# Performance work log

Measured on AMD Instinct MI355X. Metric: run time of the kernel, lower is better.

Reference implementation:

```python
import jax, jax.numpy as jnp
import numpy as np

HEADS = 16
DHEAD = 128
B, S, DMODEL = 2, 2048, 2048


def setup_inputs() -> dict:
    key = jax.random.key(0)
    k1, k2, k3 = jax.random.split(key, 3)
    x = jax.random.normal(k1, (B, S, DMODEL), dtype=jnp.float32)
    # Linear weights, stored as [in, out] so forward is x @ w (no bias).
    w_in = jax.random.normal(k2, (DMODEL, 3 * HEADS * DHEAD), dtype=jnp.float32) * (DMODEL ** -0.5)
    w_out = jax.random.normal(k3, (HEADS * DHEAD, DMODEL), dtype=jnp.float32) * ((HEADS * DHEAD) ** -0.5)
    # Causal mask: True = masked (strictly upper triangular), broadcast over batch & heads.
    mask = jnp.triu(jnp.ones((S, S), dtype=jnp.bool_), k=1)[None, None, :, :]
    return {"x": x, "w_in": w_in, "w_out": w_out, "mask": mask}


def reference(x, w_in, w_out, mask):
    b, s, _ = x.shape
    # Fused QKV projection: [b,s,3*H*dh] -> [b,s,H,3*dh] -> chunk into q,k,v [b,s,H,dh]
    projected = (x @ w_in).reshape(b, s, HEADS, 3 * DHEAD)
    q, k, v = jnp.split(projected, 3, axis=-1)
    # Scores [b,H,l,L], scaled by 1/sqrt(dhead)
    scale = 1.0 / (DHEAD ** 0.5)
    a = jnp.einsum("blhd,bLhd->bhlL", q, k) * scale
    a = jnp.where(mask, -jnp.inf, a)
    a = jax.nn.softmax(a, axis=-1)
    # Weighted values -> [b,l,H,dh] -> flatten heads -> output projection
    out = jnp.einsum("bhlL,bLhd->blhd", a, v).reshape(b, s, HEADS * DHEAD)
    return out @ w_out
```

## Files before the change

### kernel.cpp

```cpp
#include <hip/hip_runtime.h>

#define HD    16
#define DH    128
#define BB    2
#define SS    2048
#define DM    2048
#define NQKV  6144
#define MTOT  4096

typedef short   bfx8  __attribute__((ext_vector_type(8)));
typedef float   f32x4 __attribute__((ext_vector_type(4)));

__device__ __forceinline__ unsigned short f2bf(float f) {
  union { float f; unsigned int u; } c; c.f = f;
  unsigned int u = c.u + 0x7FFFu + ((c.u >> 16) & 1u);
  return (unsigned short)(u >> 16);
}

__device__ __forceinline__ void gload_lds16(const unsigned short* g, unsigned short* l) {
  __builtin_amdgcn_global_load_lds(
      (const __attribute__((address_space(1))) unsigned int*)g,
      (__attribute__((address_space(3))) unsigned int*)l, 16, 0, 0);
}

#define BARS() do { __builtin_amdgcn_sched_barrier(0); __builtin_amdgcn_s_barrier(); \
                    __builtin_amdgcn_sched_barrier(0); } while (0)
#define VMCNT7() do { asm volatile("s_waitcnt vmcnt(7)" ::: "memory"); \
                      __builtin_amdgcn_sched_barrier(0); } while (0)
#define VMCNT6() do { asm volatile("s_waitcnt vmcnt(6)" ::: "memory"); \
                      __builtin_amdgcn_sched_barrier(0); } while (0)

__global__ __launch_bounds__(256) void f32_to_bf16_k(const float* __restrict__ in,
                                                     unsigned short* __restrict__ out, int n4) {
  int i = (blockIdx.x * 256 + threadIdx.x);
  if (i >= n4) return;
  const float4 v = *(const float4*)(in + (size_t)i * 4);
  ushort4 o;
  o.x = f2bf(v.x); o.y = f2bf(v.y); o.z = f2bf(v.z); o.w = f2bf(v.w);
  *(ushort4*)(out + (size_t)i * 4) = o;
}

__global__ __launch_bounds__(256) void transpose_f32_bf16_k(const float* __restrict__ in,
                                                            unsigned short* __restrict__ out,
                                                            int R, int C) {
  __shared__ float t[32][33];
  const int c0 = blockIdx.x * 32, r0 = blockIdx.y * 32;
  const int tx = threadIdx.x & 31, ty = threadIdx.x >> 5;
#pragma unroll
  for (int i = 0; i < 4; i++) {
    int r = r0 + ty + i * 8;
    t[ty + i * 8][tx] = in[(size_t)r * C + c0 + tx];
  }
  __syncthreads();
#pragma unroll
  for (int i = 0; i < 4; i++) {
    int c = c0 + ty + i * 8;
    out[(size_t)c * R + r0 + tx] = f2bf(t[tx][ty + i * 8]);
  }
}

__global__ __launch_bounds__(512, 2) void gemm256_qkv_k(const unsigned short* __restrict__ A,
                                                        const unsigned short* __restrict__ Bt,
                                                        unsigned short* __restrict__ Qg,
                                                        unsigned short* __restrict__ Kg,
                                                        unsigned short* __restrict__ Vg,
                                                        int K) {
  __shared__ __align__(16) unsigned short Asb[2][256 * 64];
  __shared__ __align__(16) unsigned short Bsb[2][192 * 64];
  const int tid = threadIdx.x;
  const int lane = tid & 63, wid = tid >> 6;
  const int wr = wid >> 2, wc = wid & 3;
  const int cbase = lane & 15, rgrp = lane >> 4;
  const int bid = (int)blockIdx.x;
  const int id = (bid & 7) * 64 + (bid >> 3);
  const int nb = id >> 4, mb = id & 15;
  const size_t m0 = (size_t)mb * 256, n0 = (size_t)nb * 192;
  const int nkt = K >> 6;

#define STAGE_A64(u_, g_) do {                                                          \
    const int uc_ = ((u_) < nkt ? (u_) : (nkt - 1));                                    \
    const int r_ = tid >> 3, s_ = tid & 7;                                              \
    gload_lds16(A + (m0 + (g_) * 64 + r_) * (size_t)K + uc_ * 64 +                      \
                    (((s_ * 16) ^ ((r_ & 7) << 4)) >> 1),                               \
                &Asb[(u_) & 1][(g_) * 4096] + tid * 8); } while (0)
#define STAGE_B64(u_, g_) do {                                                          \
    const int uc_ = ((u_) < nkt ? (u_) : (nkt - 1));                                    \
    const int r_ = tid >> 3, s_ = tid & 7;                                              \
    gload_lds16(Bt + (n0 + (g_) * 64 + r_) * (size_t)K + uc_ * 64 +                     \
                    (((s_ * 16) ^ ((r_ & 7) << 4)) >> 1),                               \
                &Bsb[(u_) & 1][(g_) * 4096] + tid * 8); } while (0)

  const int axor = (cbase & 7) << 4;
  int a_off[2], b_off[2];
#pragma unroll
  for (int ks = 0; ks < 2; ks++) {
    a_off[ks] = ((wr * 128 + cbase) * 128 + ((ks * 64 + rgrp * 16) ^ axor)) >> 1;
    b_off[ks] = ((wc * 48 + cbase) * 128 + ((ks * 64 + rgrp * 16) ^ axor)) >> 1;
  }

#define RD_A03(dst_, p_) do { _Pragma("unroll")                                          \
    for (int mf_ = 0; mf_ < 4; mf_++) { _Pragma("unroll")                                \
      for (int ks_ = 0; ks_ < 2; ks_++)                                                  \
        dst_[mf_][ks_] = *(const bfx8*)((p_) + a_off[ks_] + mf_ * 1024); } } while (0)
#define RD_A47(dst_, p_) do { _Pragma("unroll")                                          \
    for (int mf_ = 0; mf_ < 4; mf_++) { _Pragma("unroll")                                \
      for (int ks_ = 0; ks_ < 2; ks_++)                                                  \
        dst_[mf_][ks_] = *(const bfx8*)((p_) + a_off[ks_] + (mf_ + 4) * 1024); } } while (0)
#define RD_B01(dst_, p_) do { _Pragma("unroll")                                          \
    for (int nf_ = 0; nf_ < 2; nf_++) { _Pragma("unroll")                                \
      for (int ks_ = 0; ks_ < 2; ks_++)                                                  \
        dst_[nf_][ks_] = *(const bfx8*)((p_) + b_off[ks_] + nf_ * 1024); } } while (0)
#define RD_B2(dst_, p_) do { _Pragma("unroll")                                           \
    for (int ks_ = 0; ks_ < 2; ks_++)                                                    \
      dst_[0][ks_] = *(const bfx8*)((p_) + b_off[ks_] + 2 * 1024); } while (0)

#define MFMA_2N(mo_, AF_, BF_) do {                                                      \
    __builtin_amdgcn_s_setprio(1);                                                      \
    _Pragma("unroll")                                                                    \
    for (int mf_ = 0; mf_ < 4; mf_++) { _Pragma("unroll")                                \
      for (int nf_ = 0; nf_ < 2; nf_++) { _Pragma("unroll")                              \
        for (int ks_ = 0; ks_ < 2; ks_++)                                                \
          acc[mf_ + (mo_)][nf_] = __builtin_amdgcn_mfma_f32_16x16x32_bf16(               \
              AF_[mf_][ks_], BF_[nf_][ks_], acc[mf_ + (mo_)][nf_], 0, 0, 0); } }         \
    __builtin_amdgcn_s_setprio(0); } while (0)

  f32x4 acc[8][3];
  const f32x4 z = {0.f, 0.f, 0.f, 0.f};
#pragma unroll
  for (int mf = 0; mf < 8; mf++)
#pragma unroll
    for (int nf = 0; nf < 3; nf++) acc[mf][nf] = z;

  STAGE_A64(0, 0); STAGE_A64(0, 1); STAGE_A64(0, 2); STAGE_A64(0, 3);
  STAGE_B64(0, 0); STAGE_B64(0, 1); STAGE_B64(0, 2);
  STAGE_A64(1, 0); STAGE_A64(1, 1); STAGE_A64(1, 2); STAGE_A64(1, 3);
  STAGE_B64(1, 0); STAGE_B64(1, 1); STAGE_B64(1, 2);
  VMCNT7();
  BARS();
  bfx8 a03A[4][2], b01A[2][2], a03B[4][2], b01B[2][2];
  RD_A03(a03A, &Asb[0][0]);
  RD_B01(b01A, &Bsb[0][0]);

#define TILE_BODY(u_, A03c, B01c, A03n, B01n) do {                                       \
    const unsigned short* As_  = &Asb[(u_) & 1][0];                                      \
    const unsigned short* Bs_  = &Bsb[(u_) & 1][0];                                      \
    const unsigned short* Asn_ = &Asb[((u_) + 1) & 1][0];                                \
    const unsigned short* Bsn_ = &Bsb[((u_) + 1) & 1][0];                                \
    bfx8 a47[4][2], b2[1][2];                                                            \
    RD_A47(a47, As_);                                                                    \
    STAGE_A64((u_) + 2, 0); STAGE_A64((u_) + 2, 2);                                      \
    BARS();                                                                              \
    MFMA_2N(0, A03c, B01c);                                                              \
    RD_B2(b2, Bs_);                                                                      \
    STAGE_A64((u_) + 2, 1); STAGE_A64((u_) + 2, 3);                                      \
    BARS();                                                                              \
    MFMA_2N(4, a47, B01c);                                                               \
    STAGE_B64((u_) + 2, 0); STAGE_B64((u_) + 2, 1); STAGE_B64((u_) + 2, 2);              \
    VMCNT7();                                                                            \
    BARS();                                                                              \
    RD_A03(A03n, Asn_);                                                                  \
    RD_B01(B01n, Bsn_);                                                                  \
    __builtin_amdgcn_s_setprio(1);                                                      \
    _Pragma("unroll")                                                                    \
    for (int mf_ = 0; mf_ < 4; mf_++) { _Pragma("unroll")                                \
      for (int ks_ = 0; ks_ < 2; ks_++) {                                                \
        acc[mf_][2] = __builtin_amdgcn_mfma_f32_16x16x32_bf16(                           \
            A03c[mf_][ks_], b2[0][ks_], acc[mf_][2], 0, 0, 0);                           \
        acc[mf_ + 4][2] = __builtin_amdgcn_mfma_f32_16x16x32_bf16(                       \
            a47[mf_][ks_], b2[0][ks_], acc[mf_ + 4][2], 0, 0, 0);                        \
      } }                                                                                \
    __builtin_amdgcn_s_setprio(0);                                                      \
    BARS();                                                                              \
  } while (0)

#pragma unroll 1
  for (int u = 0; u < nkt; u += 2) {
    TILE_BODY(u,     a03A, b01A, a03B, b01B);
    TILE_BODY(u + 1, a03B, b01B, a03A, b01A);
  }
#undef TILE_BODY
#undef STAGE_A64
#undef STAGE_B64

#pragma unroll
  for (int mf = 0; mf < 8; mf++)
#pragma unroll
    for (int nf = 0; nf < 3; nf++) {
      const int nn = (int)n0 + wc * 48 + nf * 16;
      const int h = nn / 384, tt = (nn >> 7) % 3;
      const int d = (nn & 127) + cbase;
      const int row0 = (int)m0 + wr * 128 + mf * 16 + rgrp * 4;
      const int bb = row0 >> 11;
      const int s0 = row0 & 2047;
      if (tt == 2) {
        ushort4 v;
        v.x = f2bf(acc[mf][nf][0]); v.y = f2bf(acc[mf][nf][1]);
        v.z = f2bf(acc[mf][nf][2]); v.w = f2bf(acc[mf][nf][3]);
        *(ushort4*)(Vg + ((size_t)(bb * HD + h) * DH + d) * SS + s0) = v;
      } else {
        unsigned short* dst = (tt == 0 ? Qg : Kg);
#pragma unroll
        for (int r = 0; r < 4; r++)
          dst[((size_t)(bb * HD + h) * SS + s0 + r) * DH + d] = f2bf(acc[mf][nf][r]);
      }
    }
}

__global__ __launch_bounds__(512, 2) void gemm256_out_k(const unsigned short* __restrict__ A,
                                                        const unsigned short* __restrict__ Bt,
                                                        float* __restrict__ C, int K, int ldc) {
  __shared__ __align__(16) unsigned short Asb[2][256 * 64];
  __shared__ __align__(16) unsigned short Bsb[2][128 * 64];
  const int tid = threadIdx.x;
  const int lane = tid & 63, wid = tid >> 6;
  const int wr = wid >> 2, wc = wid & 3;
  const int cbase = lane & 15, rgrp = lane >> 4;
  const int bid = (int)blockIdx.x;
  const int id = (bid & 7) * 32 + (bid >> 3);
  const int nb = id >> 4, mb = id & 15;
  const size_t m0 = (size_t)mb * 256, n0 = (size_t)nb * 128;
  const int nkt = K >> 6;

#define STAGE_AO(u_, g_) do {                                                           \
    const int uc_ = ((u_) < nkt ? (u_) : (nkt - 1));                                    \
    const int r_ = tid >> 3, s_ = tid & 7;                                              \
    gload_lds16(A + (m0 + (g_) * 64 + r_) * (size_t)K + uc_ * 64 +                      \
                    (((s_ * 16) ^ ((r_ & 7) << 4)) >> 1),                               \
                &Asb[(u_) & 1][(g_) * 4096] + tid * 8); } while (0)
#define STAGE_BO(u_, g_) do {                                                           \
    const int uc_ = ((u_) < nkt ? (u_) : (nkt - 1));                                    \
    const int r_ = tid >> 3, s_ = tid & 7;                                              \
    gload_lds16(Bt + (n0 + (g_) * 64 + r_) * (size_t)K + uc_ * 64 +                     \
                    (((s_ * 16) ^ ((r_ & 7) << 4)) >> 1),                               \
                &Bsb[(u_) & 1][(g_) * 4096] + tid * 8); } while (0)

  const int axor = (cbase & 7) << 4;
  int a_off[2], b_off[2];
#pragma unroll
  for (int ks = 0; ks < 2; ks++) {
    a_off[ks] = ((wr * 128 + cbase) * 128 + ((ks * 64 + rgrp * 16) ^ axor)) >> 1;
    b_off[ks] = ((wc * 32 + cbase) * 128 + ((ks * 64 + rgrp * 16) ^ axor)) >> 1;
  }

#define MFMA_O(mo_, AF_, BF_) do {                                                       \
    __builtin_amdgcn_s_setprio(1);                                                      \
    _Pragma("unroll")                                                                    \
    for (int mf_ = 0; mf_ < 4; mf_++) { _Pragma("unroll")                                \
      for (int nf_ = 0; nf_ < 2; nf_++) { _Pragma("unroll")                              \
        for (int ks_ = 0; ks_ < 2; ks_++)                                                \
          acc[mf_ + (mo_)][nf_] = __builtin_amdgcn_mfma_f32_16x16x32_bf16(               \
              AF_[mf_][ks_], BF_[nf_][ks_], acc[mf_ + (mo_)][nf_], 0, 0, 0); } }         \
    __builtin_amdgcn_s_setprio(0); } while (0)

  f32x4 acc[8][2];
  const f32x4 z = {0.f, 0.f, 0.f, 0.f};
#pragma unroll
  for (int mf = 0; mf < 8; mf++)
#pragma unroll
    for (int nf = 0; nf < 2; nf++) acc[mf][nf] = z;

  STAGE_AO(0, 0); STAGE_AO(0, 1); STAGE_AO(0, 2); STAGE_AO(0, 3);
  STAGE_BO(0, 0); STAGE_BO(0, 1);
  STAGE_AO(1, 0); STAGE_AO(1, 1); STAGE_AO(1, 2); STAGE_AO(1, 3);
  STAGE_BO(1, 0); STAGE_BO(1, 1);
  VMCNT6();
  BARS();
  bfx8 a03A[4][2], b01A[2][2], a03B[4][2], b01B[2][2];
  RD_A03(a03A, &Asb[0][0]);
  RD_B01(b01A, &Bsb[0][0]);

#define TILE_BODY_O(u_, A03c, B01c, A03n, B01n) do {                                     \
    const unsigned short* As_  = &Asb[(u_) & 1][0];                                      \
    const unsigned short* Bs_  = &Bsb[(u_) & 1][0];                                      \
    const unsigned short* Asn_ = &Asb[((u_) + 1) & 1][0];                                \
    const unsigned short* Bsn_ = &Bsb[((u_) + 1) & 1][0];                                \
    bfx8 a47[4][2];                                                                      \
    \
    RD_A47(a47, As_);                                                                    \
    STAGE_AO((u_) + 2, 0); STAGE_AO((u_) + 2, 2);                                        \
    BARS();                                                                              \
    MFMA_O(0, A03c, B01c);                                                               \
     \
               \
    STAGE_AO((u_) + 2, 1); STAGE_AO((u_) + 2, 3);                                        \
    STAGE_BO((u_) + 2, 0); STAGE_BO((u_) + 2, 1);                                        \
    VMCNT6();                                                                            \
    BARS();                                                                              \
    RD_A03(A03n, Asn_);                                                                  \
    RD_B01(B01n, Bsn_);                                                                  \
    MFMA_O(4, a47, B01c);                                                                \
    BARS();                                                                              \
  } while (0)

#pragma unroll 1
  for (int u = 0; u < nkt; u += 2) {
    TILE_BODY_O(u,     a03A, b01A, a03B, b01B);
    TILE_BODY_O(u + 1, a03B, b01B, a03A, b01A);
  }
#undef TILE_BODY_O
#undef STAGE_AO
#undef STAGE_BO

#pragma unroll
  for (int mf = 0; mf < 8; mf++)
#pragma unroll
    for (int nf = 0; nf < 2; nf++)
#pragma unroll
      for (int r = 0; r < 4; r++) {
        size_t row = m0 + wr * 128 + mf * 16 + rgrp * 4 + r;
        size_t col = n0 + wc * 32 + nf * 16 + cbase;
        C[row * ldc + col] = acc[mf][nf][r];
      }
}

__global__ __launch_bounds__(256) void attn_fwd_k(const unsigned short* __restrict__ Qg,
                                                  const unsigned short* __restrict__ Kg,
                                                  const unsigned short* __restrict__ Vg,
                                                  unsigned short* __restrict__ ao) {
  __shared__ __align__(16) unsigned short Klds[2][64 * 128];
  __shared__ __align__(16) unsigned short Vt[2][128 * 64];
  __shared__ __align__(16) unsigned short Plds[4][16 * 64];
  const int tid = threadIdx.x;
  const int lane = tid & 63, wid = tid >> 6;
  const int cbase = lane & 15, rgrp = lane >> 4;
  const int cx = (cbase & 7) << 4;

  const int bid = (int)blockIdx.x;
  const int bh = (bid & 7) * 4 + ((bid >> 3) & 3);
  const int qt = 31 - (bid >> 5);
  const int b = bh >> 4, h = bh & 15;
  const int qbase = qt * 64;

  const unsigned short* qp0 = Qg + (size_t)(b * HD + h) * SS * DH;
  const unsigned short* kp  = Kg + (size_t)(b * HD + h) * SS * DH;
  const unsigned short* vp  = Vg + (size_t)(b * HD + h) * DH * SS;
  const float scale = 0.08838834764831845f;
  const f32x4 z = {0.f, 0.f, 0.f, 0.f};
  const int qi = qbase + wid * 16 + cbase;

  bfx8 qf[4];
  {
    const unsigned short* qp = qp0 + (size_t)qi * DH;
#pragma unroll
    for (int ks = 0; ks < 4; ks++) qf[ks] = *(const bfx8*)(qp + ks * 32 + rgrp * 8);
  }

  float m_run = -1e30f, l_run = 0.f;
  f32x4 o[8];
#pragma unroll
  for (int mb = 0; mb < 8; mb++) o[mb] = z;

#define STAGE_T(t_, s_) do {                                                        \
    const int kvb_ = (t_) * 64;                                                     \
    _Pragma("unroll")                                                               \
    for (int i_ = 0; i_ < 4; i_++) {                                                \
      int idx_ = i_ * 256 + tid;                                                    \
      int r_ = idx_ >> 4, bo_ = (idx_ & 15) * 16;                                   \
      gload_lds16(kp + (size_t)(kvb_ + r_) * DH + ((bo_ ^ ((r_ & 7) << 4)) >> 1),   \
                  &Klds[s_][idx_ * 8]);                                             \
    }                                                                               \
    _Pragma("unroll")                                                               \
    for (int i_ = 0; i_ < 4; i_++) {                                                \
      int idx_ = i_ * 256 + tid;                                                    \
      int d_ = idx_ >> 3, bo_ = (idx_ & 7) * 16;                                    \
      gload_lds16(vp + (size_t)d_ * SS + kvb_ + ((bo_ ^ ((d_ & 7) << 4)) >> 1),     \
                  &Vt[s_][idx_ * 8]);                                               \
    } } while (0)

  const int ntiles = qt + 1;
  STAGE_T(0, 0);
  __syncthreads();

  for (int t = 0; t < ntiles; ++t) {
    const int sel = t & 1;
    if (t + 1 < ntiles) STAGE_T(t + 1, sel ^ 1);
    const unsigned short* Ks_ = &Klds[sel][0];
    const unsigned short* Vs_ = &Vt[sel][0];
    const int kvb = t * 64;

    f32x4 s[4];
#pragma unroll
    for (int mf = 0; mf < 4; mf++) s[mf] = z;
#pragma unroll
    for (int mf = 0; mf < 4; mf++)
#pragma unroll
      for (int ks = 0; ks < 4; ks++) {
        bfx8 kf = *(const bfx8*)(Ks_ + (((mf * 16 + cbase) * 256 + ((ks * 64 + rgrp * 16) ^ cx)) >> 1));
        s[mf] = __builtin_amdgcn_mfma_f32_16x16x32_bf16(kf, qf[ks], s[mf], 0, 0, 0);
      }

    float sv[4][4];
    const bool diag = (t == ntiles - 1);
#pragma unroll
    for (int mf = 0; mf < 4; mf++)
#pragma unroll
      for (int r = 0; r < 4; r++) {
        float v = s[mf][r] * scale;
        if (diag && (kvb + mf * 16 + rgrp * 4 + r > qi)) v = -1e30f;
        sv[mf][r] = v;
      }
    float tm = sv[0][0];
#pragma unroll
    for (int mf = 0; mf < 4; mf++)
#pragma unroll
      for (int r = 0; r < 4; r++) tm = fmaxf(tm, sv[mf][r]);
    tm = fmaxf(tm, __shfl_xor(tm, 16));
    tm = fmaxf(tm, __shfl_xor(tm, 32));
    const float mnew = fmaxf(m_run, tm);
    float p[4][4];
    float rs = 0.f;
#pragma unroll
    for (int mf = 0; mf < 4; mf++)
#pragma unroll
      for (int r = 0; r < 4; r++) { p[mf][r] = __expf(sv[mf][r] - mnew); rs += p[mf][r]; }
    rs += __shfl_xor(rs, 16);
    rs += __shfl_xor(rs, 32);
    const float alpha = __expf(m_run - mnew);
    l_run = l_run * alpha + rs;
    m_run = mnew;
#pragma unroll
    for (int mb = 0; mb < 8; mb++)
#pragma unroll
      for (int r = 0; r < 4; r++) o[mb][r] *= alpha;

#pragma unroll
    for (int mf = 0; mf < 4; mf++)
#pragma unroll
      for (int rr = 0; rr < 2; rr++) {
        unsigned int pp = (unsigned int)f2bf(p[mf][2 * rr]) |
                          ((unsigned int)f2bf(p[mf][2 * rr + 1]) << 16);
        *(unsigned int*)((char*)&Plds[wid][0] +
                         (cbase * 128 + ((mf * 32 + rgrp * 8 + rr * 4) ^ cx))) = pp;
      }
    bfx8 pf[2];
#pragma unroll
    for (int k2 = 0; k2 < 2; k2++)
      pf[k2] = *(const bfx8*)((const char*)&Plds[wid][0] +
                              (cbase * 128 + ((k2 * 64 + rgrp * 16) ^ cx)));

#pragma unroll
    for (int mb = 0; mb < 8; mb++)
#pragma unroll
      for (int k2 = 0; k2 < 2; k2++) {
        bfx8 vf = *(const bfx8*)(Vs_ + (((mb * 16 + cbase) * 128 + ((k2 * 64 + rgrp * 16) ^ cx)) >> 1));
        o[mb] = __builtin_amdgcn_mfma_f32_16x16x32_bf16(vf, pf[k2], o[mb], 0, 0, 0);
      }
    __syncthreads();
  }
#undef STAGE_T

  const float rinv = 1.0f / l_run;
  unsigned short* aop = ao + ((size_t)(b * SS + qi)) * DM + h * DH + rgrp * 4;
#pragma unroll
  for (int mb = 0; mb < 8; mb++) {
    ushort4 v;
    v.x = f2bf(o[mb][0] * rinv); v.y = f2bf(o[mb][1] * rinv);
    v.z = f2bf(o[mb][2] * rinv); v.w = f2bf(o[mb][3] * rinv);
    *(ushort4*)(aop + mb * 16) = v;
  }
}

extern "C" void kernel_launch(void* const* d_in, const int* in_sizes, int n_in,
                              void* d_out, int out_size, void* d_ws, size_t ws_size,
                              hipStream_t stream) {
  (void)in_sizes; (void)n_in; (void)out_size; (void)ws_size;
  const float* x     = (const float*)d_in[0];
  const float* w_in  = (const float*)d_in[1];
  const float* w_out = (const float*)d_in[2];
  float* out = (float*)d_out;

  char* ws = (char*)d_ws;
  unsigned short* Xb  = (unsigned short*)(ws);
  unsigned short* Wit = (unsigned short*)(ws + (16ull << 20));
  unsigned short* Wot = (unsigned short*)(ws + (40ull << 20));
  unsigned short* Qg  = (unsigned short*)(ws + (48ull << 20));
  unsigned short* Kg  = (unsigned short*)(ws + (64ull << 20));
  unsigned short* Vg  = (unsigned short*)(ws + (80ull << 20));
  unsigned short* AO  = (unsigned short*)(ws + (96ull << 20));

  f32_to_bf16_k<<<MTOT * DM / 4 / 256, 256, 0, stream>>>(x, Xb, MTOT * DM / 4);
  transpose_f32_bf16_k<<<dim3(NQKV / 32, DM / 32), 256, 0, stream>>>(w_in, Wit, DM, NQKV);
  transpose_f32_bf16_k<<<dim3(DM / 32, DM / 32), 256, 0, stream>>>(w_out, Wot, DM, DM);
  gemm256_qkv_k<<<512, 512, 0, stream>>>(Xb, Wit, Qg, Kg, Vg, DM);
  attn_fwd_k<<<1024, 256, 0, stream>>>(Qg, Kg, Vg, AO);
  gemm256_out_k<<<256, 512, 0, stream>>>(AO, Wot, out, DM, DM);
}
```

Before: 235.2 us.

## Process 128 query rows per attention block, two 16-row groups per wave

The attention kernel now handles a 128-row query tile per block, with each wave computing two 16-row query groups that share every K and V fragment read from LDS. This halves the number of blocks and the K/V global-to-LDS staging per query row, and doubles MFMA work per LDS fragment load. Waves skip KV tiles past their own causal boundary, and masking is applied per group. The cost is roughly double the accumulator registers (launch bounds now request 2 blocks per SM), fewer blocks for load balancing, and some waves idling at the diagonal tiles.

```diff
diff --git a/kernel.cpp b/kernel.cpp
--- a/kernel.cpp
+++ b/kernel.cpp
@@ -275,13 +275,10 @@
     const unsigned short* Asn_ = &Asb[((u_) + 1) & 1][0];                                \
     const unsigned short* Bsn_ = &Bsb[((u_) + 1) & 1][0];                                \
     bfx8 a47[4][2];                                                                      \
-    \
     RD_A47(a47, As_);                                                                    \
     STAGE_AO((u_) + 2, 0); STAGE_AO((u_) + 2, 2);                                        \
     BARS();                                                                              \
     MFMA_O(0, A03c, B01c);                                                               \
-     \
-               \
     STAGE_AO((u_) + 2, 1); STAGE_AO((u_) + 2, 3);                                        \
     STAGE_BO((u_) + 2, 0); STAGE_BO((u_) + 2, 1);                                        \
     VMCNT6();                                                                            \
@@ -313,13 +310,13 @@
       }
 }
 
-__global__ __launch_bounds__(256) void attn_fwd_k(const unsigned short* __restrict__ Qg,
-                                                  const unsigned short* __restrict__ Kg,
-                                                  const unsigned short* __restrict__ Vg,
-                                                  unsigned short* __restrict__ ao) {
+__global__ __launch_bounds__(256, 2) void attn_fwd_k(const unsigned short* __restrict__ Qg,
+                                                     const unsigned short* __restrict__ Kg,
+                                                     const unsigned short* __restrict__ Vg,
+                                                     unsigned short* __restrict__ ao) {
   __shared__ __align__(16) unsigned short Klds[2][64 * 128];
   __shared__ __align__(16) unsigned short Vt[2][128 * 64];
-  __shared__ __align__(16) unsigned short Plds[4][16 * 64];
+  __shared__ __align__(16) unsigned short Plds[4][2][16 * 64];
   const int tid = threadIdx.x;
   const int lane = tid & 63, wid = tid >> 6;
   const int cbase = lane & 15, rgrp = lane >> 4;
@@ -327,28 +324,36 @@
 
   const int bid = (int)blockIdx.x;
   const int bh = (bid & 7) * 4 + ((bid >> 3) & 3);
-  const int qt = 31 - (bid >> 5);
+  const int qt = 15 - (bid >> 5);
   const int b = bh >> 4, h = bh & 15;
-  const int qbase = qt * 64;
+  const int qbase = qt * 128;
 
   const unsigned short* qp0 = Qg + (size_t)(b * HD + h) * SS * DH;
   const unsigned short* kp  = Kg + (size_t)(b * HD + h) * SS * DH;
   const unsigned short* vp  = Vg + (size_t)(b * HD + h) * DH * SS;
   const float scale = 0.08838834764831845f;
   const f32x4 z = {0.f, 0.f, 0.f, 0.f};
-  const int qi = qbase + wid * 16 + cbase;
-
-  bfx8 qf[4];
-  {
-    const unsigned short* qp = qp0 + (size_t)qi * DH;
-#pragma unroll
-    for (int ks = 0; ks < 4; ks++) qf[ks] = *(const bfx8*)(qp + ks * 32 + rgrp * 8);
-  }
-
-  float m_run = -1e30f, l_run = 0.f;
-  f32x4 o[8];
-#pragma unroll
-  for (int mb = 0; mb < 8; mb++) o[mb] = z;
+  const int q0 = qbase + wid * 32;
+  const int qend = q0 + 32;
+  int qi[2];
+  qi[0] = q0 + cbase; qi[1] = q0 + 16 + cbase;
+
+  bfx8 qf[2][4];
+#pragma unroll
+  for (int g = 0; g < 2; g++) {
+    const unsigned short* qp = qp0 + (size_t)qi[g] * DH;
+#pragma unroll
+    for (int ks = 0; ks < 4; ks++) qf[g][ks] = *(const bfx8*)(qp + ks * 32 + rgrp * 8);
+  }
+
+  float m_run[2], l_run[2];
+  f32x4 o[2][8];
+#pragma unroll
+  for (int g = 0; g < 2; g++) {
+    m_run[g] = -1e30f; l_run[g] = 0.f;
+#pragma unroll
+    for (int mb = 0; mb < 8; mb++) o[g][mb] = z;
+  }
 
 #define STAGE_T(t_, s_) do {                                                        \
     const int kvb_ = (t_) * 64;                                                     \
@@ -367,7 +372,7 @@
                   &Vt[s_][idx_ * 8]);                                               \
     } } while (0)
 
-  const int ntiles = qt + 1;
+  const int ntiles = (qbase >> 6) + 2;
   STAGE_T(0, 0);
   __syncthreads();
 
@@ -378,85 +383,100 @@
     const unsigned short* Vs_ = &Vt[sel][0];
     const int kvb = t * 64;
 
-    f32x4 s[4];
-#pragma unroll
-    for (int mf = 0; mf < 4; mf++) s[mf] = z;
-#pragma unroll
-    for (int mf = 0; mf < 4; mf++)
-#pragma unroll
-      for (int ks = 0; ks < 4; ks++) {
-        bfx8 kf = *(const bfx8*)(Ks_ + (((mf * 16 + cbase) * 256 + ((ks * 64 + rgrp * 16) ^ cx)) >> 1));
-        s[mf] = __builtin_amdgcn_mfma_f32_16x16x32_bf16(kf, qf[ks], s[mf], 0, 0, 0);
+    if (kvb < qend) {
+      f32x4 s[2][4];
+#pragma unroll
+      for (int g = 0; g < 2; g++)
+#pragma unroll
+        for (int mf = 0; mf < 4; mf++) s[g][mf] = z;
+#pragma unroll
+      for (int mf = 0; mf < 4; mf++)
+#pragma unroll
+        for (int ks = 0; ks < 4; ks++) {
+          bfx8 kf = *(const bfx8*)(Ks_ + (((mf * 16 + cbase) * 256 + ((ks * 64 + rgrp * 16) ^ cx)) >> 1));
+          s[0][mf] = __builtin_amdgcn_mfma_f32_16x16x32_bf16(kf, qf[0][ks], s[0][mf], 0, 0, 0);
+          s[1][mf] = __builtin_amdgcn_mfma_f32_16x16x32_bf16(kf, qf[1][ks], s[1][mf], 0, 0, 0);
+        }
+
+      float p[2][4][4];
+#pragma unroll
+      for (int g = 0; g < 2; g++) {
+        float sv[4][4];
+        const bool maskable = (kvb + 64 > q0 + g * 16);
+#pragma unroll
+        for (int mf = 0; mf < 4; mf++)
+#pragma unroll
+          for (int r = 0; r < 4; r++) {
+            float v = s[g][mf][r] * scale;
+            if (maskable && (kvb + mf * 16 + rgrp * 4 + r > qi[g])) v = -1e30f;
+            sv[mf][r] = v;
+          }
+        float tm = sv[0][0];
+#pragma unroll
+        for (int mf = 0; mf < 4; mf++)
+#pragma unroll
+          for (int r = 0; r < 4; r++) tm = fmaxf(tm, sv[mf][r]);
+        tm = fmaxf(tm, __shfl_xor(tm, 16));
+        tm = fmaxf(tm, __shfl_xor(tm, 32));
+        const float mnew = fmaxf(m_run[g], tm);
+        float rs = 0.f;
+#pragma unroll
+        for (int mf = 0; mf < 4; mf++)
+#pragma unroll
+          for (int r = 0; r < 4; r++) { p[g][mf][r] = __expf(sv[mf][r] - mnew); rs += p[g][mf][r]; }
+        rs += __shfl_xor(rs, 16);
+        rs += __shfl_xor(rs, 32);
+        const float alpha = __expf(m_run[g] - mnew);
+        l_run[g] = l_run[g] * alpha + rs;
+        m_run[g] = mnew;
+#pragma unroll
+        for (int mb = 0; mb < 8; mb++)
+#pragma unroll
+          for (int r = 0; r < 4; r++) o[g][mb][r] *= alpha;
       }
 
-    float sv[4][4];
-    const bool diag = (t == ntiles - 1);
-#pragma unroll
-    for (int mf = 0; mf < 4; mf++)
-#pragma unroll
-      for (int r = 0; r < 4; r++) {
-        float v = s[mf][r] * scale;
-        if (diag && (kvb + mf * 16 + rgrp * 4 + r > qi)) v = -1e30f;
-        sv[mf][r] = v;
+      bfx8 pf[2][2];
+#pragma unroll
+      for (int g = 0; g < 2; g++) {
+        char* pb = (char*)&Plds[wid][g][0];
+#pragma unroll
+        for (int mf = 0; mf < 4; mf++)
+#pragma unroll
+          for (int rr = 0; rr < 2; rr++) {
+            unsigned int pp = (unsigned int)f2bf(p[g][mf][2 * rr]) |
+                              ((unsigned int)f2bf(p[g][mf][2 * rr + 1]) << 16);
+            *(unsigned int*)(pb + (cbase * 128 + ((mf * 32 + rgrp * 8 + rr * 4) ^ cx))) = pp;
+          }
+#pragma unroll
+        for (int k2 = 0; k2 < 2; k2++)
+          pf[g][k2] = *(const bfx8*)((const char*)&Plds[wid][g][0] +
+                                     (cbase * 128 + ((k2 * 64 + rgrp * 16) ^ cx)));
       }
-    float tm = sv[0][0];
-#pragma unroll
-    for (int mf = 0; mf < 4; mf++)
-#pragma unroll
-      for (int r = 0; r < 4; r++) tm = fmaxf(tm, sv[mf][r]);
-    tm = fmaxf(tm, __shfl_xor(tm, 16));
-    tm = fmaxf(tm, __shfl_xor(tm, 32));
-    const float mnew = fmaxf(m_run, tm);
-    float p[4][4];
-    float rs = 0.f;
-#pragma unroll
-    for (int mf = 0; mf < 4; mf++)
-#pragma unroll
-      for (int r = 0; r < 4; r++) { p[mf][r] = __expf(sv[mf][r] - mnew); rs += p[mf][r]; }
-    rs += __shfl_xor(rs, 16);
-    rs += __shfl_xor(rs, 32);
-    const float alpha = __expf(m_run - mnew);
-    l_run = l_run * alpha + rs;
-    m_run = mnew;
-#pragma unroll
-    for (int mb = 0; mb < 8; mb++)
-#pragma unroll
-      for (int r = 0; r < 4; r++) o[mb][r] *= alpha;
-
-#pragma unroll
-    for (int mf = 0; mf < 4; mf++)
-#pragma unroll
-      for (int rr = 0; rr < 2; rr++) {
-        unsigned int pp = (unsigned int)f2bf(p[mf][2 * rr]) |
-                          ((unsigned int)f2bf(p[mf][2 * rr + 1]) << 16);
-        *(unsigned int*)((char*)&Plds[wid][0] +
-                         (cbase * 128 + ((mf * 32 + rgrp * 8 + rr * 4) ^ cx))) = pp;
-      }
-    bfx8 pf[2];
-#pragma unroll
-    for (int k2 = 0; k2 < 2; k2++)
-      pf[k2] = *(const bfx8*)((const char*)&Plds[wid][0] +
-                              (cbase * 128 + ((k2 * 64 + rgrp * 16) ^ cx)));
-
-#pragma unroll
-    for (int mb = 0; mb < 8; mb++)
-#pragma unroll
-      for (int k2 = 0; k2 < 2; k2++) {
-        bfx8 vf = *(const bfx8*)(Vs_ + (((mb * 16 + cbase) * 128 + ((k2 * 64 + rgrp * 16) ^ cx)) >> 1));
-        o[mb] = __builtin_amdgcn_mfma_f32_16x16x32_bf16(vf, pf[k2], o[mb], 0, 0, 0);
-      }
+
+#pragma unroll
+      for (int mb = 0; mb < 8; mb++)
+#pragma unroll
+        for (int k2 = 0; k2 < 2; k2++) {
+          bfx8 vf = *(const bfx8*)(Vs_ + (((mb * 16 + cbase) * 128 + ((k2 * 64 + rgrp * 16) ^ cx)) >> 1));
+          o[0][mb] = __builtin_amdgcn_mfma_f32_16x16x32_bf16(vf, pf[0][k2], o[0][mb], 0, 0, 0);
+          o[1][mb] = __builtin_amdgcn_mfma_f32_16x16x32_bf16(vf, pf[1][k2], o[1][mb], 0, 0, 0);
+        }
+    }
     __syncthreads();
   }
 #undef STAGE_T
 
-  const float rinv = 1.0f / l_run;
-  unsigned short* aop = ao + ((size_t)(b * SS + qi)) * DM + h * DH + rgrp * 4;
-#pragma unroll
-  for (int mb = 0; mb < 8; mb++) {
-    ushort4 v;
-    v.x = f2bf(o[mb][0] * rinv); v.y = f2bf(o[mb][1] * rinv);
-    v.z = f2bf(o[mb][2] * rinv); v.w = f2bf(o[mb][3] * rinv);
-    *(ushort4*)(aop + mb * 16) = v;
+#pragma unroll
+  for (int g = 0; g < 2; g++) {
+    const float rinv = 1.0f / l_run[g];
+    unsigned short* aop = ao + ((size_t)(b * SS + qi[g])) * DM + h * DH + rgrp * 4;
+#pragma unroll
+    for (int mb = 0; mb < 8; mb++) {
+      ushort4 v;
+      v.x = f2bf(o[g][mb][0] * rinv); v.y = f2bf(o[g][mb][1] * rinv);
+      v.z = f2bf(o[g][mb][2] * rinv); v.w = f2bf(o[g][mb][3] * rinv);
+      *(ushort4*)(aop + mb * 16) = v;
+    }
   }
 }
 
@@ -482,6 +502,6 @@
   transpose_f32_bf16_k<<<dim3(NQKV / 32, DM / 32), 256, 0, stream>>>(w_in, Wit, DM, NQKV);
   transpose_f32_bf16_k<<<dim3(DM / 32, DM / 32), 256, 0, stream>>>(w_out, Wot, DM, DM);
   gemm256_qkv_k<<<512, 512, 0, stream>>>(Xb, Wit, Qg, Kg, Vg, DM);
-  attn_fwd_k<<<1024, 256, 0, stream>>>(Qg, Kg, Vg, AO);
+  attn_fwd_k<<<512, 256, 0, stream>>>(Qg, Kg, Vg, AO);
   gemm256_out_k<<<256, 512, 0, stream>>>(AO, Wot, out, DM, DM);
 }
```

Result: slower. 249.0 us (+5.9%).

## Reshape QKV GEMM wave grid to 4x2 with 64x96 per-wave tiles

Applied to the files above, without the earlier changes.

Changes the QKV projection GEMM's wave layout from 2x4 waves (128x48 per wave) to 4x2 waves (64x96 per wave), and restructures the inner tile loop to hold all A fragments and stream B fragments in three pairs. Each wave now reads 64 rows of A and 96 columns of B per k-step instead of 128 and 48, which changes LDS read volume per MFMA and the interleaving of staging, barriers and MFMA phases. The read macros for the output-projection GEMM are moved below so that kernel still compiles. Register pressure and the overlap between LDS reads and MFMAs shift, which could help or hurt.

```diff
diff --git a/kernel.cpp b/kernel.cpp
--- a/kernel.cpp
+++ b/kernel.cpp
@@ -69,7 +69,7 @@
   __shared__ __align__(16) unsigned short Bsb[2][192 * 64];
   const int tid = threadIdx.x;
   const int lane = tid & 63, wid = tid >> 6;
-  const int wr = wid >> 2, wc = wid & 3;
+  const int wr = wid >> 1, wc = wid & 1;
   const int cbase = lane & 15, rgrp = lane >> 4;
   const int bid = (int)blockIdx.x;
   const int id = (bid & 7) * 64 + (bid >> 3);
@@ -94,42 +94,35 @@
   int a_off[2], b_off[2];
 #pragma unroll
   for (int ks = 0; ks < 2; ks++) {
-    a_off[ks] = ((wr * 128 + cbase) * 128 + ((ks * 64 + rgrp * 16) ^ axor)) >> 1;
-    b_off[ks] = ((wc * 48 + cbase) * 128 + ((ks * 64 + rgrp * 16) ^ axor)) >> 1;
-  }
-
-#define RD_A03(dst_, p_) do { _Pragma("unroll")                                          \
+    a_off[ks] = ((wr * 64 + cbase) * 128 + ((ks * 64 + rgrp * 16) ^ axor)) >> 1;
+    b_off[ks] = ((wc * 96 + cbase) * 128 + ((ks * 64 + rgrp * 16) ^ axor)) >> 1;
+  }
+
+#define RD_AALL(dst_, p_) do { _Pragma("unroll")                                         \
     for (int mf_ = 0; mf_ < 4; mf_++) { _Pragma("unroll")                                \
       for (int ks_ = 0; ks_ < 2; ks_++)                                                  \
         dst_[mf_][ks_] = *(const bfx8*)((p_) + a_off[ks_] + mf_ * 1024); } } while (0)
-#define RD_A47(dst_, p_) do { _Pragma("unroll")                                          \
-    for (int mf_ = 0; mf_ < 4; mf_++) { _Pragma("unroll")                                \
-      for (int ks_ = 0; ks_ < 2; ks_++)                                                  \
-        dst_[mf_][ks_] = *(const bfx8*)((p_) + a_off[ks_] + (mf_ + 4) * 1024); } } while (0)
-#define RD_B01(dst_, p_) do { _Pragma("unroll")                                          \
+#define RD_BP(dst_, p_, P_) do { _Pragma("unroll")                                       \
     for (int nf_ = 0; nf_ < 2; nf_++) { _Pragma("unroll")                                \
       for (int ks_ = 0; ks_ < 2; ks_++)                                                  \
-        dst_[nf_][ks_] = *(const bfx8*)((p_) + b_off[ks_] + nf_ * 1024); } } while (0)
-#define RD_B2(dst_, p_) do { _Pragma("unroll")                                           \
-    for (int ks_ = 0; ks_ < 2; ks_++)                                                    \
-      dst_[0][ks_] = *(const bfx8*)((p_) + b_off[ks_] + 2 * 1024); } while (0)
-
-#define MFMA_2N(mo_, AF_, BF_) do {                                                      \
+        dst_[nf_][ks_] = *(const bfx8*)((p_) + b_off[ks_] + (nf_ + (P_)) * 1024); } } while (0)
+
+#define MFMA_P(no_, AF_, BF_) do {                                                       \
     __builtin_amdgcn_s_setprio(1);                                                      \
     _Pragma("unroll")                                                                    \
     for (int mf_ = 0; mf_ < 4; mf_++) { _Pragma("unroll")                                \
       for (int nf_ = 0; nf_ < 2; nf_++) { _Pragma("unroll")                              \
         for (int ks_ = 0; ks_ < 2; ks_++)                                                \
-          acc[mf_ + (mo_)][nf_] = __builtin_amdgcn_mfma_f32_16x16x32_bf16(               \
-              AF_[mf_][ks_], BF_[nf_][ks_], acc[mf_ + (mo_)][nf_], 0, 0, 0); } }         \
+          acc[mf_][nf_ + (no_)] = __builtin_amdgcn_mfma_f32_16x16x32_bf16(               \
+              AF_[mf_][ks_], BF_[nf_][ks_], acc[mf_][nf_ + (no_)], 0, 0, 0); } }         \
     __builtin_amdgcn_s_setprio(0); } while (0)
 
-  f32x4 acc[8][3];
+  f32x4 acc[4][6];
   const f32x4 z = {0.f, 0.f, 0.f, 0.f};
 #pragma unroll
-  for (int mf = 0; mf < 8; mf++)
-#pragma unroll
-    for (int nf = 0; nf < 3; nf++) acc[mf][nf] = z;
+  for (int mf = 0; mf < 4; mf++)
+#pragma unroll
+    for (int nf = 0; nf < 6; nf++) acc[mf][nf] = z;
 
   STAGE_A64(0, 0); STAGE_A64(0, 1); STAGE_A64(0, 2); STAGE_A64(0, 3);
   STAGE_B64(0, 0); STAGE_B64(0, 1); STAGE_B64(0, 2);
@@ -137,59 +130,54 @@
   STAGE_B64(1, 0); STAGE_B64(1, 1); STAGE_B64(1, 2);
   VMCNT7();
   BARS();
-  bfx8 a03A[4][2], b01A[2][2], a03B[4][2], b01B[2][2];
-  RD_A03(a03A, &Asb[0][0]);
-  RD_B01(b01A, &Bsb[0][0]);
-
-#define TILE_BODY(u_, A03c, B01c, A03n, B01n) do {                                       \
-    const unsigned short* As_  = &Asb[(u_) & 1][0];                                      \
+  bfx8 aA[4][2], b01A[2][2], aB[4][2], b01B[2][2];
+  RD_AALL(aA, &Asb[0][0]);
+  RD_BP(b01A, &Bsb[0][0], 0);
+
+#define TILE_BODY(u_, Ac, B01c, An, B01n) do {                                           \
     const unsigned short* Bs_  = &Bsb[(u_) & 1][0];                                      \
     const unsigned short* Asn_ = &Asb[((u_) + 1) & 1][0];                                \
     const unsigned short* Bsn_ = &Bsb[((u_) + 1) & 1][0];                                \
-    bfx8 a47[4][2], b2[1][2];                                                            \
-    RD_A47(a47, As_);                                                                    \
-    STAGE_A64((u_) + 2, 0); STAGE_A64((u_) + 2, 2);                                      \
-    BARS();                                                                              \
-    MFMA_2N(0, A03c, B01c);                                                              \
-    RD_B2(b2, Bs_);                                                                      \
-    STAGE_A64((u_) + 2, 1); STAGE_A64((u_) + 2, 3);                                      \
-    BARS();                                                                              \
-    MFMA_2N(4, a47, B01c);                                                               \
-    STAGE_B64((u_) + 2, 0); STAGE_B64((u_) + 2, 1); STAGE_B64((u_) + 2, 2);              \
+    bfx8 b23[2][2], b45[2][2];                                                           \
+                   \
+    RD_BP(b23, Bs_, 2);                                                                  \
+    STAGE_A64((u_) + 2, 0); STAGE_A64((u_) + 2, 1);                                      \
+    STAGE_A64((u_) + 2, 2); STAGE_A64((u_) + 2, 3);                                      \
+    BARS();                                                                              \
+    MFMA_P(0, Ac, B01c);                                                                 \
+                   \
+    RD_BP(b45, Bs_, 4);                                                                  \
+    STAGE_B64((u_) + 2, 0);                                                              \
+    BARS();                                                                              \
+    MFMA_P(2, Ac, b23);                                                                  \
+       \
+                                                \
+    STAGE_B64((u_) + 2, 1); STAGE_B64((u_) + 2, 2);                                      \
     VMCNT7();                                                                            \
     BARS();                                                                              \
-    RD_A03(A03n, Asn_);                                                                  \
-    RD_B01(B01n, Bsn_);                                                                  \
-    __builtin_amdgcn_s_setprio(1);                                                      \
-    _Pragma("unroll")                                                                    \
-    for (int mf_ = 0; mf_ < 4; mf_++) { _Pragma("unroll")                                \
-      for (int ks_ = 0; ks_ < 2; ks_++) {                                                \
-        acc[mf_][2] = __builtin_amdgcn_mfma_f32_16x16x32_bf16(                           \
-            A03c[mf_][ks_], b2[0][ks_], acc[mf_][2], 0, 0, 0);                           \
-        acc[mf_ + 4][2] = __builtin_amdgcn_mfma_f32_16x16x32_bf16(                       \
-            a47[mf_][ks_], b2[0][ks_], acc[mf_ + 4][2], 0, 0, 0);                        \
-      } }                                                                                \
-    __builtin_amdgcn_s_setprio(0);                                                      \
+    RD_AALL(An, Asn_);                                                                   \
+    RD_BP(B01n, Bsn_, 0);                                                                \
+    MFMA_P(4, Ac, b45);                                                                  \
     BARS();                                                                              \
   } while (0)
 
 #pragma unroll 1
   for (int u = 0; u < nkt; u += 2) {
-    TILE_BODY(u,     a03A, b01A, a03B, b01B);
-    TILE_BODY(u + 1, a03B, b01B, a03A, b01A);
+    TILE_BODY(u,     aA, b01A, aB, b01B);
+    TILE_BODY(u + 1, aB, b01B, aA, b01A);
   }
 #undef TILE_BODY
 #undef STAGE_A64
 #undef STAGE_B64
 
 #pragma unroll
-  for (int mf = 0; mf < 8; mf++)
-#pragma unroll
-    for (int nf = 0; nf < 3; nf++) {
-      const int nn = (int)n0 + wc * 48 + nf * 16;
+  for (int mf = 0; mf < 4; mf++)
+#pragma unroll
+    for (int nf = 0; nf < 6; nf++) {
+      const int nn = (int)n0 + wc * 96 + nf * 16;
       const int h = nn / 384, tt = (nn >> 7) % 3;
       const int d = (nn & 127) + cbase;
-      const int row0 = (int)m0 + wr * 128 + mf * 16 + rgrp * 4;
+      const int row0 = (int)m0 + wr * 64 + mf * 16 + rgrp * 4;
       const int bb = row0 >> 11;
       const int s0 = row0 & 2047;
       if (tt == 2) {
@@ -242,6 +230,19 @@
     b_off[ks] = ((wc * 32 + cbase) * 128 + ((ks * 64 + rgrp * 16) ^ axor)) >> 1;
   }
 
+#define RD_A03(dst_, p_) do { _Pragma("unroll")                                          \
+    for (int mf_ = 0; mf_ < 4; mf_++) { _Pragma("unroll")                                \
+      for (int ks_ = 0; ks_ < 2; ks_++)                                                  \
+        dst_[mf_][ks_] = *(const bfx8*)((p_) + a_off[ks_] + mf_ * 1024); } } while (0)
+#define RD_A47(dst_, p_) do { _Pragma("unroll")                                          \
+    for (int mf_ = 0; mf_ < 4; mf_++) { _Pragma("unroll")                                \
+      for (int ks_ = 0; ks_ < 2; ks_++)                                                  \
+        dst_[mf_][ks_] = *(const bfx8*)((p_) + a_off[ks_] + (mf_ + 4) * 1024); } } while (0)
+#define RD_B01(dst_, p_) do { _Pragma("unroll")                                          \
+    for (int nf_ = 0; nf_ < 2; nf_++) { _Pragma("unroll")                                \
+      for (int ks_ = 0; ks_ < 2; ks_++)                                                  \
+        dst_[nf_][ks_] = *(const bfx8*)((p_) + b_off[ks_] + nf_ * 1024); } } while (0)
+
 #define MFMA_O(mo_, AF_, BF_) do {                                                       \
     __builtin_amdgcn_s_setprio(1);                                                      \
     _Pragma("unroll")                                                                    \
@@ -271,17 +272,13 @@
 
 #define TILE_BODY_O(u_, A03c, B01c, A03n, B01n) do {                                     \
     const unsigned short* As_  = &Asb[(u_) & 1][0];                                      \
-    const unsigned short* Bs_  = &Bsb[(u_) & 1][0];                                      \
     const unsigned short* Asn_ = &Asb[((u_) + 1) & 1][0];                                \
     const unsigned short* Bsn_ = &Bsb[((u_) + 1) & 1][0];                                \
     bfx8 a47[4][2];                                                                      \
-    \
     RD_A47(a47, As_);                                                                    \
     STAGE_AO((u_) + 2, 0); STAGE_AO((u_) + 2, 2);                                        \
     BARS();                                                                              \
     MFMA_O(0, A03c, B01c);                                                               \
-     \
-               \
     STAGE_AO((u_) + 2, 1); STAGE_AO((u_) + 2, 3);                                        \
     STAGE_BO((u_) + 2, 0); STAGE_BO((u_) + 2, 1);                                        \
     VMCNT6();                                                                            \
```

Result: no change. 232.6 us (-1.1%).
